# Optimization experiments

Hardware: AMD Instinct MI355X
Metric: run time of the kernel (lower is better)

## Reference

```python
import jax, jax.numpy as jnp
import numpy as np

NH = 8  # n_heads
LN_EPS = 1e-5

def _ln(x, g, b):
    m = x.mean(-1, keepdims=True)
    v = ((x - m) ** 2).mean(-1, keepdims=True)
    return (x - m) / jnp.sqrt(v + LN_EPS) * g + b

def _l2norm(x):
    n = jnp.sqrt(jnp.sum(x * x, axis=-1, keepdims=True))
    return x / jnp.maximum(n, 1e-12)

def _block(h, inw, inb, outw, outb, g1, b1, g2, b2, w1, bb1, w2, bb2):
    B, T, D = h.shape
    hd = D // NH
    res = h
    hn = _ln(h, g1, b1)
    qkv = hn @ inw.T + inb
    q, k, v = jnp.split(qkv, 3, axis=-1)
    q = q.reshape(B, T, NH, hd)
    k = k.reshape(B, T, NH, hd)
    v = v.reshape(B, T, NH, hd)
    scores = jnp.einsum('bthd,bshd->bhts', q, k) / jnp.sqrt(jnp.asarray(hd, h.dtype))
    a = jax.nn.softmax(scores, axis=-1)
    o = jnp.einsum('bhts,bshd->bthd', a, v).reshape(B, T, D)
    h = res + o @ outw.T + outb
    f = _ln(h, g2, b2)
    f = jax.nn.gelu(f @ w1.T + bb1, approximate=False) @ w2.T + bb2
    return h + f

def setup_inputs() -> dict:
    B, T, IN, D, L, NS, NP = 8, 1024, 1024, 512, 4, 1024, 512
    key = jax.random.key(0)
    ks = jax.random.split(key, 24)
    gn = jax.random.normal
    u = jax.random.uniform(ks[1], (B, T, NS), dtype=jnp.float32, minval=1e-6, maxval=1.0 - 1e-6)
    gumbel = -jnp.log(-jnp.log(u))
    s = lambda fan: 1.0 / np.sqrt(fan)
    inp = {
        'x': gn(ks[0], (B, T, IN), dtype=jnp.float32),
        'gumbel': gumbel,
        'sym_w': gn(ks[2], (D, IN)) * s(IN),
        'sym_b': jnp.zeros((D,)),
        'codebook': gn(ks[3], (NS, D)) * 0.1,
        'pos_enc': gn(ks[4], (1, 2000, D)) * 0.02,
        'attn_in_w': gn(ks[5], (L, 3 * D, D)) * s(D),
        'attn_in_b': jnp.zeros((L, 3 * D)),
        'attn_out_w': gn(ks[6], (L, D, D)) * s(D),
        'attn_out_b': jnp.zeros((L, D)),
        'n1_g': jnp.ones((L, D)), 'n1_b': jnp.zeros((L, D)),
        'n2_g': jnp.ones((L, D)), 'n2_b': jnp.zeros((L, D)),
        'ffn_w1': gn(ks[7], (L, 4 * D, D)) * s(D),
        'ffn_b1': jnp.zeros((L, 4 * D)),
        'ffn_w2': gn(ks[8], (L, D, 4 * D)) * s(4 * D),
        'ffn_b2': jnp.zeros((L, D)),
        'q_w': gn(ks[9], (D, D)) * s(D),
        'q_b': jnp.zeros((D,)),
        'qln_g': jnp.ones((D,)), 'qln_b': jnp.zeros((D,)),
        'patterns': gn(ks[10], (NP, D)) * s(D),
        'epoch': 0,
        'total_epochs': 100,
    }
    return inp

def reference(x, gumbel, sym_w, sym_b, codebook, pos_enc,
              attn_in_w, attn_in_b, attn_out_w, attn_out_b,
              n1_g, n1_b, n2_g, n2_b, ffn_w1, ffn_b1, ffn_w2, ffn_b2,
              q_w, q_b, qln_g, qln_b, patterns, epoch, total_epochs):
    B, T, _ = x.shape
    # SymbolizationLayer (soft, gumbel-softmax with tau=0.5)
    hp = x @ sym_w.T + sym_b                               # [B,T,D]
    logits_s = _l2norm(hp) @ _l2norm(codebook).T / 0.5     # [B,T,NS]
    soft = jax.nn.softmax((logits_s + gumbel) / 0.5, axis=-1)
    h = soft @ codebook + pos_enc[:, :T, :]
    # transformer blocks
    for i in range(attn_in_w.shape[0]):
        h = _block(h, attn_in_w[i], attn_in_b[i], attn_out_w[i], attn_out_b[i],
                   n1_g[i], n1_b[i], n2_g[i], n2_b[i],
                   ffn_w1[i], ffn_b1[i], ffn_w2[i], ffn_b2[i])
    # VQPatternMatrix (eval mode: hard assignments, no EMA updates)
    Q = _l2norm(_ln(h @ q_w.T + q_b, qln_g, qln_b))
    temp = max(0.5, 1.0 - 0.5 * epoch / total_epochs)
    logits = Q @ _l2norm(patterns).T / temp                # [B,T,NP]
    hard_idx = jnp.argmax(logits, axis=-1)                 # [B,T]
    assign = jax.nn.one_hot(hard_idx, patterns.shape[0], dtype=logits.dtype)
    emb = jnp.take(patterns, hard_idx, axis=0)             # gather = one_hot @ patterns
    return (emb, assign, logits, h, hard_idx)
```

## Files before the change

kernel.cpp:

```cpp
#include <hip/hip_runtime.h>

#define DEV __device__ __forceinline__

typedef unsigned short u16;
typedef unsigned int u32;
typedef __attribute__((ext_vector_type(8))) _Float16 h8_t;
typedef __attribute__((ext_vector_type(4))) float f4_t;

constexpr int T_SEQ = 1024;
constexpr int DMODEL = 512;
constexpr int NPAT = 512;

enum {
  E_BIAS = 0,
  E_VQ = 5,
  E_RES = 6,
  E_POS = 8,
  E_GUM2 = 9,
  E_GELU2 = 10,
  E_QKV2 = 11
};

DEV float h2f(u16 h) { return (float)__builtin_bit_cast(_Float16, h); }
DEV void split2(float x, u16& h, u16& l) {
  _Float16 hh = (_Float16)x;
  float r = x - (float)hh;
  _Float16 ll = (_Float16)r;
  h = __builtin_bit_cast(u16, hh);
  l = __builtin_bit_cast(u16, ll);
}

DEV f4_t mfh(h8_t a, h8_t b, f4_t c) {
  return __builtin_amdgcn_mfma_f32_16x16x32_f16(a, b, c, 0, 0, 0);
}
DEV f4_t prod3(h8_t ah, h8_t al, h8_t bh, h8_t bl, f4_t c) {
  c = mfh(ah, bh, c);
  c = mfh(ah, bl, c);
  c = mfh(al, bh, c);
  return c;
}

typedef const __attribute__((address_space(1))) unsigned char* gas_t;
typedef __attribute__((address_space(3))) unsigned char* las_t;
DEV void gload16(const u16* g, u16* l) {
  __builtin_amdgcn_global_load_lds((gas_t)(const void*)g, (las_t)(void*)l, 16,
                                   0, 0);
}

template <int EPI>
__global__ __launch_bounds__(256, 2) void gemm_mf(
    const u16* __restrict__ Ah, const u16* __restrict__ Al,
    const u16* __restrict__ Bh, const u16* __restrict__ Bl,
    const float* __restrict__ bias, const float* __restrict__ res,
    float* __restrict__ Cf, u16* __restrict__ Ch, u16* __restrict__ Cl, int N,
    int KK, int lda, int ldb, int gx) {
  __shared__ __align__(16) u16 AsH[2][128][4][8], AsL[2][128][4][8];
  __shared__ __align__(16) u16 BsH[2][128][4][8], BsL[2][128][4][8];
  const int tid = threadIdx.x;
  const int w = tid >> 6, lane = tid & 63;
  const int wy = w >> 1, wx = w & 1;
  const int lr = lane & 15, lg = lane >> 4;

  const int nwg = gridDim.x;
  const int bid = blockIdx.x;
  const int qq = nwg >> 3;
  const int wg = (bid & 7) * qq + (bid >> 3);
  const int by = wg / gx, bx = wg % gx;
  const int bm = by * 128, bn = bx * 128;

  const int rowl = lane >> 2, slot4 = lane & 3;

  auto STAGE = [&](int k0, int buf) {
#pragma unroll
    for (int it = 0; it < 4; ++it) {
      const int f = w + 4 * it;
      const int plane = f >> 3;
      const int ch = f & 7;
      const int row = ch * 16 + rowl;
      const int kp = slot4 ^ ((row >> 1) & 3);
      const size_t g = (size_t)(bm + row) * lda + k0 + kp * 8;
      if (plane == 0)
        gload16(&Ah[g], &AsH[buf][0][0][0] + ch * 512);
      else
        gload16(&Al[g], &AsL[buf][0][0][0] + ch * 512);
    }
#pragma unroll
    for (int it = 0; it < 4; ++it) {
      const int f = w + 4 * it;
      const int plane = f >> 3;
      const int ch = f & 7;
      const int row = ch * 16 + rowl;
      const int kp = slot4 ^ ((row >> 1) & 3);
      const size_t g = (size_t)(bn + row) * ldb + k0 + kp * 8;
      if (plane == 0)
        gload16(&Bh[g], &BsH[buf][0][0][0] + ch * 512);
      else
        gload16(&Bl[g], &BsL[buf][0][0][0] + ch * 512);
    }
  };

  f4_t acc[4][4];
#pragma unroll
  for (int mt = 0; mt < 4; ++mt)
#pragma unroll
    for (int nt = 0; nt < 4; ++nt) acc[mt][nt] = (f4_t){0.f, 0.f, 0.f, 0.f};

  const int nsteps = KK / 32;
  STAGE(0, 0);
  __syncthreads();
  for (int t = 0; t < nsteps; ++t) {
    const int cur = t & 1;
    if (t + 1 < nsteps) STAGE((t + 1) * 32, cur ^ 1);

    h8_t fah[4], fal[4], fbh[4], fbl[4];
#pragma unroll
    for (int mt = 0; mt < 4; ++mt) {
      int row = wy * 64 + mt * 16 + lr;
      int slot = lg ^ ((row >> 1) & 3);
      fah[mt] = *(const h8_t*)&AsH[cur][row][slot][0];
      fal[mt] = *(const h8_t*)&AsL[cur][row][slot][0];
    }
#pragma unroll
    for (int nt = 0; nt < 4; ++nt) {
      int col = wx * 64 + nt * 16 + lr;
      int slot = lg ^ ((col >> 1) & 3);
      fbh[nt] = *(const h8_t*)&BsH[cur][col][slot][0];
      fbl[nt] = *(const h8_t*)&BsL[cur][col][slot][0];
    }
#pragma unroll
    for (int mt = 0; mt < 4; ++mt)
#pragma unroll
      for (int nt = 0; nt < 4; ++nt)
        acc[mt][nt] = prod3(fah[mt], fal[mt], fbh[nt], fbl[nt], acc[mt][nt]);
    __syncthreads();
  }

  float bv[4];
  if constexpr (EPI == E_BIAS || EPI == E_RES || EPI == E_GELU2 ||
                EPI == E_QKV2) {
#pragma unroll
    for (int nt = 0; nt < 4; ++nt) bv[nt] = bias[bn + wx * 64 + nt * 16 + lr];
  }
#pragma unroll
  for (int mt = 0; mt < 4; ++mt)
#pragma unroll
    for (int nt = 0; nt < 4; ++nt) {
      const int c = bn + wx * 64 + nt * 16 + lr;
#pragma unroll
      for (int i = 0; i < 4; ++i) {
        const int m = bm + wy * 64 + mt * 16 + 4 * lg + i;
        const size_t idx = (size_t)m * N + c;
        float v = acc[mt][nt][i];
        if constexpr (EPI == E_BIAS) {
          Cf[idx] = v + bv[nt];
        } else if constexpr (EPI == E_RES) {
          Cf[idx] = v + bv[nt] + res[idx];
        } else if constexpr (EPI == E_POS) {
          Cf[idx] = v + res[(size_t)(m & 1023) * N + c];
        } else if constexpr (EPI == E_GUM2) {
          float t = 4.0f * v + 2.0f * res[idx];
          u16 h2, l2;
          split2(t, h2, l2);
          Ch[idx] = h2;
          Cl[idx] = l2;
        } else if constexpr (EPI == E_GELU2) {
          float t = v + bv[nt];
          float g = 0.5f * t * (1.0f + erff(t * 0.7071067811865476f));
          u16 h2, l2;
          split2(g, h2, l2);
          Ch[idx] = h2;
          Cl[idx] = l2;
        } else if constexpr (EPI == E_QKV2) {
          float t = v + bv[nt];
          u16 h2, l2;
          split2(t, h2, l2);
          size_t o;
          if (c < 512) {
            o = (size_t)m * 512 + c;
          } else if (c < 1024) {
            o = 4194304 + (size_t)m * 512 + (c - 512);
          } else {
            int cc = c - 1024, hh2 = cc >> 6, dd = cc & 63;
            int bb2 = m >> 10, tt = m & 1023;
            o = 8388608 +
                (((size_t)(bb2 * 8 + hh2) * 64 + dd) << 10) + tt;
          }
          Ch[o] = h2;
          Cl[o] = l2;
        }
      }
    }
}

__global__ __launch_bounds__(256, 4) void flash_mfma(
    const u16* __restrict__ QKVh, const u16* __restrict__ QKVl,
    u16* __restrict__ Oh, u16* __restrict__ Ol) {
  __shared__ __align__(16) u16 KP[2][64][8][8];
  __shared__ __align__(16) u16 Vs[2][64][8][8];
  const int tid = threadIdx.x;
  const int w = tid >> 6, lane = tid & 63;
  const int lr = lane & 15, lg = lane >> 4;
  const int bid = blockIdx.x;
  const int b = bid & 7;
  const int slot_b = bid >> 3;
  const int hh = slot_b >> 4;
  const int qt = slot_b & 15;

  const u16* Qh = QKVh;
  const u16* Ql = QKVl;
  const u16* Kh = QKVh + 4194304;
  const u16* Kl = QKVl + 4194304;
  const u16* Vh = QKVh + 8388608;
  const u16* Vl = QKVl + 8388608;

  h8_t qf[2][2];
  {
    size_t g =
        ((size_t)(b * 1024 + qt * 64 + w * 16 + lr)) * 512 + hh * 64 + lg * 8;
    qf[0][0] = *(const h8_t*)&Qh[g];
    qf[0][1] = *(const h8_t*)&Ql[g];
    qf[1][0] = *(const h8_t*)&Qh[g + 32];
    qf[1][1] = *(const h8_t*)&Ql[g + 32];
  }

  f4_t oacc[4];
#pragma unroll
  for (int nt = 0; nt < 4; ++nt) oacc[nt] = (f4_t){0.f, 0.f, 0.f, 0.f};
  float mrun[4], lrun[4];
#pragma unroll
  for (int i = 0; i < 4; ++i) {
    mrun[i] = -__builtin_huge_valf();
    lrun[i] = 0.0f;
  }

  const int rowl8 = lane >> 3, slot8 = lane & 7;

  for (int kt = 0; kt < 16; ++kt) {
    __syncthreads();
#pragma unroll
    for (int it = 0; it < 4; ++it) {
      const int f = w + 4 * it;
      const int plane = f >> 3, ch = f & 7;
      const int row = ch * 8 + rowl8;
      const int kp = slot8 ^ (row & 7);
      const size_t gk =
          ((size_t)(b * 1024 + kt * 64 + row)) * 512 + hh * 64 + kp * 8;
      if (plane == 0)
        gload16(&Kh[gk], &KP[0][0][0][0] + ch * 512);
      else
        gload16(&Kl[gk], &KP[1][0][0][0] + ch * 512);
    }
#pragma unroll
    for (int it = 0; it < 4; ++it) {
      const int f = w + 4 * it;
      const int plane = f >> 3, ch = f & 7;
      const int row = ch * 8 + rowl8;
      const int kp = slot8 ^ (row & 7);
      const size_t gv =
          ((size_t)((b * 8 + hh) * 64 + row)) * 1024 + kt * 64 + kp * 8;
      if (plane == 0)
        gload16(&Vh[gv], &Vs[0][0][0][0] + ch * 512);
      else
        gload16(&Vl[gv], &Vs[1][0][0][0] + ch * 512);
    }
    __syncthreads();

    f4_t s[4];
#pragma unroll
    for (int nt = 0; nt < 4; ++nt) {
      s[nt] = (f4_t){0.f, 0.f, 0.f, 0.f};
      const int col = nt * 16 + lr;
#pragma unroll
      for (int ks = 0; ks < 2; ++ks) {
        int slt = (ks * 4 + lg) ^ (col & 7);
        h8_t kh = *(const h8_t*)&KP[0][col][slt][0];
        h8_t kl = *(const h8_t*)&KP[1][col][slt][0];
        s[nt] = prod3(qf[ks][0], qf[ks][1], kh, kl, s[nt]);
      }
    }

#pragma unroll
    for (int i = 0; i < 4; ++i) {
      float rm = -__builtin_huge_valf();
#pragma unroll
      for (int nt = 0; nt < 4; ++nt) {
        s[nt][i] *= 0.125f;
        rm = fmaxf(rm, s[nt][i]);
      }
      rm = fmaxf(rm, __shfl_xor(rm, 1));
      rm = fmaxf(rm, __shfl_xor(rm, 2));
      rm = fmaxf(rm, __shfl_xor(rm, 4));
      rm = fmaxf(rm, __shfl_xor(rm, 8));
      float mnew = fmaxf(mrun[i], rm);
      float alpha = __expf(mrun[i] - mnew);
      float rs = 0.0f;
#pragma unroll
      for (int nt = 0; nt < 4; ++nt) {
        float p = __expf(s[nt][i] - mnew);
        s[nt][i] = p;
        rs += p;
      }
      rs += __shfl_xor(rs, 1);
      rs += __shfl_xor(rs, 2);
      rs += __shfl_xor(rs, 4);
      rs += __shfl_xor(rs, 8);
      lrun[i] = lrun[i] * alpha + rs;
      mrun[i] = mnew;
#pragma unroll
      for (int nt = 0; nt < 4; ++nt) oacc[nt][i] *= alpha;
    }

    __syncthreads();

#pragma unroll
    for (int nt = 0; nt < 4; ++nt)
#pragma unroll
      for (int i = 0; i < 4; ++i) {
        int qrow = w * 16 + 4 * lg + i;
        int kv = nt * 16 + lr;
        int kp = kv >> 3, j = kv & 7;
        int slt = kp ^ (qrow & 7);
        u16 h2, l2;
        split2(s[nt][i], h2, l2);
        KP[0][qrow][slt][j] = h2;
        KP[1][qrow][slt][j] = l2;
      }

    h8_t pf[2][2];
#pragma unroll
    for (int ks = 0; ks < 2; ++ks) {
      int row = w * 16 + lr;
      int slt = (ks * 4 + lg) ^ (row & 7);
      pf[ks][0] = *(const h8_t*)&KP[0][row][slt][0];
      pf[ks][1] = *(const h8_t*)&KP[1][row][slt][0];
    }
#pragma unroll
    for (int ntd = 0; ntd < 4; ++ntd) {
      const int col = ntd * 16 + lr;
#pragma unroll
      for (int ks = 0; ks < 2; ++ks) {
        int slt = (ks * 4 + lg) ^ (col & 7);
        h8_t vh = *(const h8_t*)&Vs[0][col][slt][0];
        h8_t vl = *(const h8_t*)&Vs[1][col][slt][0];
        oacc[ntd] = prod3(pf[ks][0], pf[ks][1], vh, vl, oacc[ntd]);
      }
    }
  }

#pragma unroll
  for (int i = 0; i < 4; ++i) {
    float inv = 1.0f / lrun[i];
    int t = qt * 64 + w * 16 + 4 * lg + i;
#pragma unroll
    for (int ntd = 0; ntd < 4; ++ntd) {
      int d = hh * 64 + ntd * 16 + lr;
      size_t idx = ((size_t)(b * 1024 + t)) * 512 + d;
      u16 h2, l2;
      split2(oacc[ntd][i] * inv, h2, l2);
      Oh[idx] = h2;
      Ol[idx] = l2;
    }
  }
}

template <int BM, int BN, int WR, int EPI>
__global__ __launch_bounds__((BM / WR) * (BN / 64) * 64) void gemm_f32(
    const float* __restrict__ A, const float* __restrict__ Bmat,
    const float* __restrict__ bias, float* __restrict__ C, int M, int N, int K,
    const int* __restrict__ ep, const int* __restrict__ tot) {
  constexpr int BK = 16;
  constexpr int WN = BN / 64;
  constexpr int NW = (BM / WR) * WN;
  constexpr int NT = NW * 64;
  constexpr int RM = WR / 8;
  __shared__ __align__(16) float As[BK][BM + 4];
  __shared__ __align__(16) float Bs[BK][BN + 4];
  const int tid = threadIdx.x;
  const int w = tid >> 6, lane = tid & 63;
  const int wy = w / WN, wx = w % WN;
  const int ly = lane >> 3, lx = lane & 7;
  const int bm = blockIdx.y * BM;
  const int bn = blockIdx.x * BN;
  const int rbase = wy * WR + ly * RM;

  float acc[RM][8];
#pragma unroll
  for (int i = 0; i < RM; ++i)
#pragma unroll
    for (int j = 0; j < 8; ++j) acc[i][j] = 0.0f;

  for (int k0 = 0; k0 < K; k0 += BK) {
#pragma unroll
    for (int i = 0; i < (BM * BK / 4) / NT; ++i) {
      int idx = tid + i * NT;
      int r = idx >> 2, c4 = (idx & 3) << 2;
      const float4 v = *(const float4*)(A + (size_t)(bm + r) * K + k0 + c4);
      As[c4 + 0][r] = v.x;
      As[c4 + 1][r] = v.y;
      As[c4 + 2][r] = v.z;
      As[c4 + 3][r] = v.w;
    }
#pragma unroll
    for (int i = 0; i < (BN * BK / 4) / NT; ++i) {
      int idx = tid + i * NT;
      int r = idx >> 2, c4 = (idx & 3) << 2;
      const float4 v = *(const float4*)(Bmat + (size_t)(bn + r) * K + k0 + c4);
      Bs[c4 + 0][r] = v.x;
      Bs[c4 + 1][r] = v.y;
      Bs[c4 + 2][r] = v.z;
      Bs[c4 + 3][r] = v.w;
    }
    __syncthreads();
#pragma unroll
    for (int k = 0; k < BK; ++k) {
      float a[RM], b[8];
#pragma unroll
      for (int r4 = 0; r4 < RM; r4 += 4)
        *(float4*)&a[r4] = *(const float4*)&As[k][rbase + r4];
      *(float4*)&b[0] = *(const float4*)&Bs[k][wx * 64 + lx * 8];
      *(float4*)&b[4] = *(const float4*)&Bs[k][wx * 64 + lx * 8 + 4];
#pragma unroll
      for (int i = 0; i < RM; ++i)
#pragma unroll
        for (int j = 0; j < 8; ++j) acc[i][j] = fmaf(a[i], b[j], acc[i][j]);
    }
    __syncthreads();
  }

  const int ncol = bn + wx * 64 + lx * 8;
  float bb[8];
  if constexpr (EPI == E_BIAS) {
    *(float4*)&bb[0] = *(const float4*)(bias + ncol);
    *(float4*)&bb[4] = *(const float4*)(bias + ncol + 4);
  }
  float invt = 1.0f;
  if constexpr (EPI == E_VQ) {
    float t = 1.0f - 0.5f * (float)ep[0] / (float)tot[0];
    invt = 1.0f / fmaxf(0.5f, t);
  }
#pragma unroll
  for (int i = 0; i < RM; ++i) {
    const int m = bm + rbase + i;
    float o[8];
#pragma unroll
    for (int j = 0; j < 8; ++j) o[j] = acc[i][j];
    if constexpr (EPI == E_BIAS) {
#pragma unroll
      for (int j = 0; j < 8; ++j) o[j] += bb[j];
    } else if constexpr (EPI == E_VQ) {
#pragma unroll
      for (int j = 0; j < 8; ++j) o[j] *= invt;
    }
    *(float4*)(C + (size_t)m * N + ncol) = *(float4*)&o[0];
    *(float4*)(C + (size_t)m * N + ncol + 4) = *(float4*)&o[4];
  }
}

DEV float wave_sum(float v) {
#pragma unroll
  for (int off = 1; off < 64; off <<= 1) v += __shfl_xor(v, off);
  return v;
}

DEV void store8_split2(u16* H, u16* L, size_t base, const float* t) {
  u16 vh[8], vl[8];
#pragma unroll
  for (int j = 0; j < 8; ++j) split2(t[j], vh[j], vl[j]);
  *(ushort4*)&H[base] = make_ushort4(vh[0], vh[1], vh[2], vh[3]);
  *(ushort4*)&H[base + 4] = make_ushort4(vh[4], vh[5], vh[6], vh[7]);
  *(ushort4*)&L[base] = make_ushort4(vl[0], vl[1], vl[2], vl[3]);
  *(ushort4*)&L[base + 4] = make_ushort4(vl[4], vl[5], vl[6], vl[7]);
}

__global__ __launch_bounds__(256) void ln_split2(const float* __restrict__ x,
                                                 const float* __restrict__ g,
                                                 const float* __restrict__ b,
                                                 u16* __restrict__ yh,
                                                 u16* __restrict__ yl) {
  const int row = blockIdx.x * 4 + (threadIdx.x >> 6);
  const int lane = threadIdx.x & 63;
  const float* xr = x + (size_t)row * DMODEL;
  float v[8];
  *(float4*)&v[0] = *(const float4*)(xr + lane * 8);
  *(float4*)&v[4] = *(const float4*)(xr + lane * 8 + 4);
  float s = 0.0f;
#pragma unroll
  for (int j = 0; j < 8; ++j) s += v[j];
  s = wave_sum(s);
  float mean = s * (1.0f / 512.0f);
  float s2 = 0.0f;
#pragma unroll
  for (int j = 0; j < 8; ++j) {
    float d = v[j] - mean;
    s2 += d * d;
  }
  s2 = wave_sum(s2);
  float rstd = 1.0f / sqrtf(s2 * (1.0f / 512.0f) + 1e-5f);
  float gg[8], bv[8];
  *(float4*)&gg[0] = *(const float4*)(g + lane * 8);
  *(float4*)&gg[4] = *(const float4*)(g + lane * 8 + 4);
  *(float4*)&bv[0] = *(const float4*)(b + lane * 8);
  *(float4*)&bv[4] = *(const float4*)(b + lane * 8 + 4);
  float t[8];
#pragma unroll
  for (int j = 0; j < 8; ++j) t[j] = (v[j] - mean) * rstd * gg[j] + bv[j];
  store8_split2(yh, yl, (size_t)row * DMODEL + lane * 8, t);
}

__global__ __launch_bounds__(256) void ln_l2_f32(const float* __restrict__ x,
                                                 const float* __restrict__ g,
                                                 const float* __restrict__ b,
                                                 float* __restrict__ y) {
  const int row = blockIdx.x * 4 + (threadIdx.x >> 6);
  const int lane = threadIdx.x & 63;
  const float* xr = x + (size_t)row * DMODEL;
  float v[8];
  *(float4*)&v[0] = *(const float4*)(xr + lane * 8);
  *(float4*)&v[4] = *(const float4*)(xr + lane * 8 + 4);
  float s = 0.0f;
#pragma unroll
  for (int j = 0; j < 8; ++j) s += v[j];
  s = wave_sum(s);
  float mean = s * (1.0f / 512.0f);
  float s2 = 0.0f;
#pragma unroll
  for (int j = 0; j < 8; ++j) {
    float d = v[j] - mean;
    s2 += d * d;
  }
  s2 = wave_sum(s2);
  float rstd = 1.0f / sqrtf(s2 * (1.0f / 512.0f) + 1e-5f);
  float gg[8], bv[8];
  *(float4*)&gg[0] = *(const float4*)(g + lane * 8);
  *(float4*)&gg[4] = *(const float4*)(g + lane * 8 + 4);
  *(float4*)&bv[0] = *(const float4*)(b + lane * 8);
  *(float4*)&bv[4] = *(const float4*)(b + lane * 8 + 4);
  float t[8];
#pragma unroll
  for (int j = 0; j < 8; ++j) t[j] = (v[j] - mean) * rstd * gg[j] + bv[j];
  float n2 = 0.0f;
#pragma unroll
  for (int j = 0; j < 8; ++j) n2 += t[j] * t[j];
  n2 = wave_sum(n2);
  float den = fmaxf(sqrtf(n2), 1e-12f);
#pragma unroll
  for (int j = 0; j < 8; ++j) t[j] /= den;
  float* yr = y + (size_t)row * DMODEL;
  *(float4*)(yr + lane * 8) = *(float4*)&t[0];
  *(float4*)(yr + lane * 8 + 4) = *(float4*)&t[4];
}

__global__ __launch_bounds__(256) void l2_split2(const float* __restrict__ x,
                                                 u16* __restrict__ yh,
                                                 u16* __restrict__ yl) {
  const int row = blockIdx.x * 4 + (threadIdx.x >> 6);
  const int lane = threadIdx.x & 63;
  const float* xr = x + (size_t)row * DMODEL;
  float v[8];
  *(float4*)&v[0] = *(const float4*)(xr + lane * 8);
  *(float4*)&v[4] = *(const float4*)(xr + lane * 8 + 4);
  float n2 = 0.0f;
#pragma unroll
  for (int j = 0; j < 8; ++j) n2 += v[j] * v[j];
  n2 = wave_sum(n2);
  float den = fmaxf(sqrtf(n2), 1e-12f);
#pragma unroll
  for (int j = 0; j < 8; ++j) v[j] /= den;
  store8_split2(yh, yl, (size_t)row * DMODEL + lane * 8, v);
}

__global__ __launch_bounds__(256) void l2_f32(const float* __restrict__ x,
                                              float* __restrict__ y) {
  const int row = blockIdx.x * 4 + (threadIdx.x >> 6);
  const int lane = threadIdx.x & 63;
  const float* xr = x + (size_t)row * DMODEL;
  float v[8];
  *(float4*)&v[0] = *(const float4*)(xr + lane * 8);
  *(float4*)&v[4] = *(const float4*)(xr + lane * 8 + 4);
  float n2 = 0.0f;
#pragma unroll
  for (int j = 0; j < 8; ++j) n2 += v[j] * v[j];
  n2 = wave_sum(n2);
  float den = fmaxf(sqrtf(n2), 1e-12f);
#pragma unroll
  for (int j = 0; j < 8; ++j) v[j] /= den;
  float* yr = y + (size_t)row * DMODEL;
  *(float4*)(yr + lane * 8) = *(float4*)&v[0];
  *(float4*)(yr + lane * 8 + 4) = *(float4*)&v[4];
}

__global__ __launch_bounds__(256) void softmax2(u16* __restrict__ H,
                                                u16* __restrict__ L) {
  const int row = blockIdx.x;
  const int tid = threadIdx.x;
  const size_t base = (size_t)row * 1024 + tid * 4;
  ushort4 qh = *(const ushort4*)&H[base];
  ushort4 ql = *(const ushort4*)&L[base];
  float v0 = h2f(qh.x) + h2f(ql.x);
  float v1 = h2f(qh.y) + h2f(ql.y);
  float v2 = h2f(qh.z) + h2f(ql.z);
  float v3 = h2f(qh.w) + h2f(ql.w);
  float mx = fmaxf(fmaxf(v0, v1), fmaxf(v2, v3));
#pragma unroll
  for (int off = 1; off < 64; off <<= 1) mx = fmaxf(mx, __shfl_xor(mx, off));
  __shared__ float red[4];
  const int wv = tid >> 6;
  if ((tid & 63) == 0) red[wv] = mx;
  __syncthreads();
  mx = fmaxf(fmaxf(red[0], red[1]), fmaxf(red[2], red[3]));
  float e0 = __expf(v0 - mx), e1 = __expf(v1 - mx), e2 = __expf(v2 - mx),
        e3 = __expf(v3 - mx);
  float s = e0 + e1 + e2 + e3;
#pragma unroll
  for (int off = 1; off < 64; off <<= 1) s += __shfl_xor(s, off);
  __syncthreads();
  if ((tid & 63) == 0) red[wv] = s;
  __syncthreads();
  s = red[0] + red[1] + red[2] + red[3];
  float inv = 1.0f / s;
  u16 ah[4], al[4];
  split2(e0 * inv, ah[0], al[0]);
  split2(e1 * inv, ah[1], al[1]);
  split2(e2 * inv, ah[2], al[2]);
  split2(e3 * inv, ah[3], al[3]);
  *(ushort4*)&H[base] = make_ushort4(ah[0], ah[1], ah[2], ah[3]);
  *(ushort4*)&L[base] = make_ushort4(al[0], al[1], al[2], al[3]);
}

__global__ __launch_bounds__(256) void split2_k(const float* __restrict__ src,
                                                u16* __restrict__ H,
                                                u16* __restrict__ L, int n4) {
  for (int e = blockIdx.x * 256 + threadIdx.x; e < n4; e += gridDim.x * 256) {
    float4 v = *(const float4*)(src + (size_t)e * 4);
    u16 ah[4], al[4];
    split2(v.x, ah[0], al[0]);
    split2(v.y, ah[1], al[1]);
    split2(v.z, ah[2], al[2]);
    split2(v.w, ah[3], al[3]);
    *(ushort4*)&H[(size_t)e * 4] = make_ushort4(ah[0], ah[1], ah[2], ah[3]);
    *(ushort4*)&L[(size_t)e * 4] = make_ushort4(al[0], al[1], al[2], al[3]);
  }
}

__global__ __launch_bounds__(256) void tsplit_cb(const float* __restrict__ cb,
                                                 u16* __restrict__ th,
                                                 u16* __restrict__ tl) {
  const int c = blockIdx.x;
  const int t = threadIdx.x;
  u16 ah[4], al[4];
#pragma unroll
  for (int j = 0; j < 4; ++j) {
    float v = cb[(size_t)(4 * t + j) * 512 + c];
    split2(v, ah[j], al[j]);
  }
  const size_t base = (size_t)c * 1024 + 4 * t;
  *(ushort4*)&th[base] = make_ushort4(ah[0], ah[1], ah[2], ah[3]);
  *(ushort4*)&tl[base] = make_ushort4(al[0], al[1], al[2], al[3]);
}

__global__ __launch_bounds__(256) void vq_finalize(
    const float* __restrict__ logits, const float* __restrict__ patterns,
    float* __restrict__ emb, float* __restrict__ assign,
    float* __restrict__ idxf) {
  const int row = blockIdx.x * 4 + (threadIdx.x >> 6);
  const int lane = threadIdx.x & 63;
  const float* lr = logits + (size_t)row * NPAT;
  float best = -__builtin_huge_valf();
  int bi = 0;
#pragma unroll
  for (int jj = 0; jj < 8; ++jj) {
    int j = lane + jj * 64;
    float v = lr[j];
    if (v > best) {
      best = v;
      bi = j;
    }
  }
#pragma unroll
  for (int off = 1; off < 64; off <<= 1) {
    float ob = __shfl_xor(best, off);
    int oi = __shfl_xor(bi, off);
    if (ob > best || (ob == best && oi < bi)) {
      best = ob;
      bi = oi;
    }
  }
  const float* pr = patterns + (size_t)bi * DMODEL;
#pragma unroll
  for (int g = 0; g < 2; ++g) {
    int c = lane * 8 + g * 4;
    float4 pv = *(const float4*)(pr + c);
    *(float4*)(emb + (size_t)row * DMODEL + c) = pv;
    float4 av;
    av.x = (c + 0 == bi) ? 1.0f : 0.0f;
    av.y = (c + 1 == bi) ? 1.0f : 0.0f;
    av.z = (c + 2 == bi) ? 1.0f : 0.0f;
    av.w = (c + 3 == bi) ? 1.0f : 0.0f;
    *(float4*)(assign + (size_t)row * NPAT + c) = av;
  }
  if (lane == 0) idxf[row] = (float)bi;
}

extern "C" void kernel_launch(void* const* d_in, const int* in_sizes, int n_in,
                              void* d_out, int out_size, void* d_ws,
                              size_t ws_size, hipStream_t stream) {
  (void)in_sizes;
  (void)n_in;
  (void)out_size;
  (void)ws_size;
  const float* x = (const float*)d_in[0];
  const float* gumbel = (const float*)d_in[1];
  const float* sym_w = (const float*)d_in[2];
  const float* sym_b = (const float*)d_in[3];
  const float* codebook = (const float*)d_in[4];
  const float* pos_enc = (const float*)d_in[5];
  const float* attn_in_w = (const float*)d_in[6];
  const float* attn_in_b = (const float*)d_in[7];
  const float* attn_out_w = (const float*)d_in[8];
  const float* attn_out_b = (const float*)d_in[9];
  const float* n1_g = (const float*)d_in[10];
  const float* n1_b = (const float*)d_in[11];
  const float* n2_g = (const float*)d_in[12];
  const float* n2_b = (const float*)d_in[13];
  const float* ffn_w1 = (const float*)d_in[14];
  const float* ffn_b1 = (const float*)d_in[15];
  const float* ffn_w2 = (const float*)d_in[16];
  const float* ffn_b2 = (const float*)d_in[17];
  const float* q_w = (const float*)d_in[18];
  const float* q_b = (const float*)d_in[19];
  const float* qln_g = (const float*)d_in[20];
  const float* qln_b = (const float*)d_in[21];
  const float* patterns = (const float*)d_in[22];
  const int* epoch = (const int*)d_in[23];
  const int* tot = (const int*)d_in[24];

  float* out = (float*)d_out;
  float* emb = out;
  float* assign = out + 4194304;
  float* logits = out + 8388608;
  float* h = out + 12582912;
  float* idxf = out + 16777216;

  float* ws_f = (float*)d_ws;
  u16* a16 = (u16*)ws_f;
  float* bF = ws_f + 18874368;
  u16* b16 = (u16*)bF;
  u16 *hnH = b16, *hnL = b16 + 4194304;
  float* wF = ws_f + 25165824;
  u16* w16 = (u16*)wF;

  u16 *xH = a16, *xL = a16 + 8388608;
  split2_k<<<2048, 256, 0, stream>>>(x, xH, xL, 2097152);
  split2_k<<<512, 256, 0, stream>>>(sym_w, w16, w16 + 524288, 131072);
  gemm_mf<E_BIAS><<<256, 256, 0, stream>>>(xH, xL, w16, w16 + 524288, sym_b,
                                           nullptr, bF, nullptr, nullptr, 512,
                                           1024, 1024, 1024, 4);
  l2_split2<<<256, 256, 0, stream>>>(codebook, w16, w16 + 524288);
  u16 *hpH = a16, *hpL = a16 + 4194304;
  l2_split2<<<2048, 256, 0, stream>>>(bF, hpH, hpL);
  u16 *sH = a16 + 12582912, *sL = a16 + 20971520;
  gemm_mf<E_GUM2><<<512, 256, 0, stream>>>(hpH, hpL, w16, w16 + 524288,
                                           nullptr, gumbel, nullptr, sH, sL,
                                           1024, 512, 512, 512, 8);
  softmax2<<<8192, 256, 0, stream>>>(sH, sL);
  tsplit_cb<<<512, 256, 0, stream>>>(codebook, w16, w16 + 524288);
  gemm_mf<E_POS><<<256, 256, 0, stream>>>(sH, sL, w16, w16 + 524288, nullptr,
                                          pos_enc, h, nullptr, nullptr, 512,
                                          1024, 1024, 1024, 4);

  u16 *qkvH = a16, *qkvL = a16 + 12582912;
  u16* w1p = a16 + 33554432;
  u16* w2p = b16 + 8388608;
  u16 *pH = a16, *pL = a16 + 16777216;

  for (int l = 0; l < 4; ++l) {
    const float* inw = attn_in_w + (size_t)l * 1536 * 512;
    const float* inb = attn_in_b + (size_t)l * 1536;
    const float* outw = attn_out_w + (size_t)l * 512 * 512;
    const float* outb = attn_out_b + (size_t)l * 512;
    const float* w1 = ffn_w1 + (size_t)l * 2048 * 512;
    const float* b1 = ffn_b1 + (size_t)l * 2048;
    const float* w2 = ffn_w2 + (size_t)l * 512 * 2048;
    const float* b2 = ffn_b2 + (size_t)l * 512;

    ln_split2<<<2048, 256, 0, stream>>>(h, n1_g + l * 512, n1_b + l * 512,
                                        hnH, hnL);
    split2_k<<<1024, 256, 0, stream>>>(inw, w16, w16 + 786432, 196608);
    gemm_mf<E_QKV2><<<768, 256, 0, stream>>>(hnH, hnL, w16, w16 + 786432, inb,
                                             nullptr, nullptr, qkvH, qkvL,
                                             1536, 512, 512, 512, 12);
    flash_mfma<<<1024, 256, 0, stream>>>(qkvH, qkvL, hnH, hnL);
    split2_k<<<256, 256, 0, stream>>>(outw, w16, w16 + 262144, 65536);
    gemm_mf<E_RES><<<256, 256, 0, stream>>>(hnH, hnL, w16, w16 + 262144, outb,
                                            h, h, nullptr, nullptr, 512, 512,
                                            512, 512, 4);
    ln_split2<<<2048, 256, 0, stream>>>(h, n2_g + l * 512, n2_b + l * 512,
                                        hnH, hnL);
    split2_k<<<1024, 256, 0, stream>>>(w1, w1p, w1p + 1048576, 262144);
    split2_k<<<1024, 256, 0, stream>>>(w2, w2p, w2p + 1048576, 262144);
    gemm_mf<E_GELU2><<<1024, 256, 0, stream>>>(hnH, hnL, w1p, w1p + 1048576,
                                               b1, nullptr, nullptr, pH, pL,
                                               2048, 512, 512, 512, 16);
    gemm_mf<E_RES><<<256, 256, 0, stream>>>(pH, pL, w2p, w2p + 1048576, b2, h,
                                            h, nullptr, nullptr, 512, 2048,
                                            2048, 2048, 4);
  }

  gemm_f32<64, 128, 32, E_BIAS><<<dim3(4, 128), 256, 0, stream>>>(
      h, q_w, q_b, bF, 8192, 512, 512, nullptr, nullptr);
  ln_l2_f32<<<2048, 256, 0, stream>>>(bF, qln_g, qln_b, bF);
  l2_f32<<<128, 256, 0, stream>>>(patterns, wF);
  gemm_f32<64, 128, 32, E_VQ><<<dim3(4, 128), 256, 0, stream>>>(
      bF, wF, nullptr, logits, 8192, 512, 512, epoch, tot);
  vq_finalize<<<2048, 256, 0, stream>>>(logits, patterns, emb, assign, idxf);
}
```

Before: 1.766 ms.

## Use BM=64 MFMA tiles for narrow GEMMs and move VQ head onto split-fp16 MFMA

Templates the split-fp16 MFMA GEMM on row-tile height, so the N=512 GEMMs (symbolization, gumbel, pos, out-proj, FFN2) launch twice as many 64-row blocks for better CU fill. It also replaces the scalar fp32 GEMMs of the final VQ projection and pattern logits with the split-fp16 MFMA GEMM, adding split kernels and a temperature-scaling epilogue. This risks small precision differences in the logits and argmax that depend on the three-product fp16 split emulation.

```diff
diff --git a/kernel.cpp b/kernel.cpp
--- a/kernel.cpp
+++ b/kernel.cpp
@@ -47,14 +47,17 @@
                                    0, 0);
 }
 
-template <int EPI>
-__global__ __launch_bounds__(256, 2) void gemm_mf(
+template <int BM, int EPI>
+__global__ __launch_bounds__(256, BM == 64 ? 3 : 2) void gemm_mf(
     const u16* __restrict__ Ah, const u16* __restrict__ Al,
     const u16* __restrict__ Bh, const u16* __restrict__ Bl,
     const float* __restrict__ bias, const float* __restrict__ res,
     float* __restrict__ Cf, u16* __restrict__ Ch, u16* __restrict__ Cl, int N,
-    int KK, int lda, int ldb, int gx) {
-  __shared__ __align__(16) u16 AsH[2][128][4][8], AsL[2][128][4][8];
+    int KK, int lda, int ldb, int gx, const int* __restrict__ ep,
+    const int* __restrict__ tot) {
+  constexpr int MT = BM / 32;
+  constexpr int CPP = BM / 16;
+  __shared__ __align__(16) u16 AsH[2][BM][4][8], AsL[2][BM][4][8];
   __shared__ __align__(16) u16 BsH[2][128][4][8], BsL[2][128][4][8];
   const int tid = threadIdx.x;
   const int w = tid >> 6, lane = tid & 63;
@@ -66,16 +69,16 @@
   const int qq = nwg >> 3;
   const int wg = (bid & 7) * qq + (bid >> 3);
   const int by = wg / gx, bx = wg % gx;
-  const int bm = by * 128, bn = bx * 128;
+  const int bm = by * BM, bn = bx * 128;
 
   const int rowl = lane >> 2, slot4 = lane & 3;
 
   auto STAGE = [&](int k0, int buf) {
 #pragma unroll
-    for (int it = 0; it < 4; ++it) {
+    for (int it = 0; it < CPP / 2; ++it) {
       const int f = w + 4 * it;
-      const int plane = f >> 3;
-      const int ch = f & 7;
+      const int plane = f / CPP;
+      const int ch = f % CPP;
       const int row = ch * 16 + rowl;
       const int kp = slot4 ^ ((row >> 1) & 3);
       const size_t g = (size_t)(bm + row) * lda + k0 + kp * 8;
@@ -99,9 +102,9 @@
     }
   };
 
-  f4_t acc[4][4];
-#pragma unroll
-  for (int mt = 0; mt < 4; ++mt)
+  f4_t acc[MT][4];
+#pragma unroll
+  for (int mt = 0; mt < MT; ++mt)
 #pragma unroll
     for (int nt = 0; nt < 4; ++nt) acc[mt][nt] = (f4_t){0.f, 0.f, 0.f, 0.f};
 
@@ -112,10 +115,10 @@
     const int cur = t & 1;
     if (t + 1 < nsteps) STAGE((t + 1) * 32, cur ^ 1);
 
-    h8_t fah[4], fal[4], fbh[4], fbl[4];
-#pragma unroll
-    for (int mt = 0; mt < 4; ++mt) {
-      int row = wy * 64 + mt * 16 + lr;
+    h8_t fah[MT], fal[MT], fbh[4], fbl[4];
+#pragma unroll
+    for (int mt = 0; mt < MT; ++mt) {
+      int row = wy * (BM / 2) + mt * 16 + lr;
       int slot = lg ^ ((row >> 1) & 3);
       fah[mt] = *(const h8_t*)&AsH[cur][row][slot][0];
       fal[mt] = *(const h8_t*)&AsL[cur][row][slot][0];
@@ -128,7 +131,7 @@
       fbl[nt] = *(const h8_t*)&BsL[cur][col][slot][0];
     }
 #pragma unroll
-    for (int mt = 0; mt < 4; ++mt)
+    for (int mt = 0; mt < MT; ++mt)
 #pragma unroll
       for (int nt = 0; nt < 4; ++nt)
         acc[mt][nt] = prod3(fah[mt], fal[mt], fbh[nt], fbl[nt], acc[mt][nt]);
@@ -141,18 +144,25 @@
 #pragma unroll
     for (int nt = 0; nt < 4; ++nt) bv[nt] = bias[bn + wx * 64 + nt * 16 + lr];
   }
-#pragma unroll
-  for (int mt = 0; mt < 4; ++mt)
+  float invt = 1.0f;
+  if constexpr (EPI == E_VQ) {
+    float tt = 1.0f - 0.5f * (float)ep[0] / (float)tot[0];
+    invt = 1.0f / fmaxf(0.5f, tt);
+  }
+#pragma unroll
+  for (int mt = 0; mt < MT; ++mt)
 #pragma unroll
     for (int nt = 0; nt < 4; ++nt) {
       const int c = bn + wx * 64 + nt * 16 + lr;
 #pragma unroll
       for (int i = 0; i < 4; ++i) {
-        const int m = bm + wy * 64 + mt * 16 + 4 * lg + i;
+        const int m = bm + wy * (BM / 2) + mt * 16 + 4 * lg + i;
         const size_t idx = (size_t)m * N + c;
         float v = acc[mt][nt][i];
         if constexpr (EPI == E_BIAS) {
           Cf[idx] = v + bv[nt];
+        } else if constexpr (EPI == E_VQ) {
+          Cf[idx] = v * invt;
         } else if constexpr (EPI == E_RES) {
           Cf[idx] = v + bv[nt] + res[idx];
         } else if constexpr (EPI == E_POS) {
@@ -181,9 +191,9 @@
             o = 4194304 + (size_t)m * 512 + (c - 512);
           } else {
             int cc = c - 1024, hh2 = cc >> 6, dd = cc & 63;
-            int bb2 = m >> 10, tt = m & 1023;
+            int bb2 = m >> 10, tt2 = m & 1023;
             o = 8388608 +
-                (((size_t)(bb2 * 8 + hh2) * 64 + dd) << 10) + tt;
+                (((size_t)(bb2 * 8 + hh2) * 64 + dd) << 10) + tt2;
           }
           Ch[o] = h2;
           Cl[o] = l2;
@@ -363,99 +373,6 @@
   }
 }
 
-template <int BM, int BN, int WR, int EPI>
-__global__ __launch_bounds__((BM / WR) * (BN / 64) * 64) void gemm_f32(
-    const float* __restrict__ A, const float* __restrict__ Bmat,
-    const float* __restrict__ bias, float* __restrict__ C, int M, int N, int K,
-    const int* __restrict__ ep, const int* __restrict__ tot) {
-  constexpr int BK = 16;
-  constexpr int WN = BN / 64;
-  constexpr int NW = (BM / WR) * WN;
-  constexpr int NT = NW * 64;
-  constexpr int RM = WR / 8;
-  __shared__ __align__(16) float As[BK][BM + 4];
-  __shared__ __align__(16) float Bs[BK][BN + 4];
-  const int tid = threadIdx.x;
-  const int w = tid >> 6, lane = tid & 63;
-  const int wy = w / WN, wx = w % WN;
-  const int ly = lane >> 3, lx = lane & 7;
-  const int bm = blockIdx.y * BM;
-  const int bn = blockIdx.x * BN;
-  const int rbase = wy * WR + ly * RM;
-
-  float acc[RM][8];
-#pragma unroll
-  for (int i = 0; i < RM; ++i)
-#pragma unroll
-    for (int j = 0; j < 8; ++j) acc[i][j] = 0.0f;
-
-  for (int k0 = 0; k0 < K; k0 += BK) {
-#pragma unroll
-    for (int i = 0; i < (BM * BK / 4) / NT; ++i) {
-      int idx = tid + i * NT;
-      int r = idx >> 2, c4 = (idx & 3) << 2;
-      const float4 v = *(const float4*)(A + (size_t)(bm + r) * K + k0 + c4);
-      As[c4 + 0][r] = v.x;
-      As[c4 + 1][r] = v.y;
-      As[c4 + 2][r] = v.z;
-      As[c4 + 3][r] = v.w;
-    }
-#pragma unroll
-    for (int i = 0; i < (BN * BK / 4) / NT; ++i) {
-      int idx = tid + i * NT;
-      int r = idx >> 2, c4 = (idx & 3) << 2;
-      const float4 v = *(const float4*)(Bmat + (size_t)(bn + r) * K + k0 + c4);
-      Bs[c4 + 0][r] = v.x;
-      Bs[c4 + 1][r] = v.y;
-      Bs[c4 + 2][r] = v.z;
-      Bs[c4 + 3][r] = v.w;
-    }
-    __syncthreads();
-#pragma unroll
-    for (int k = 0; k < BK; ++k) {
-      float a[RM], b[8];
-#pragma unroll
-      for (int r4 = 0; r4 < RM; r4 += 4)
-        *(float4*)&a[r4] = *(const float4*)&As[k][rbase + r4];
-      *(float4*)&b[0] = *(const float4*)&Bs[k][wx * 64 + lx * 8];
-      *(float4*)&b[4] = *(const float4*)&Bs[k][wx * 64 + lx * 8 + 4];
-#pragma unroll
-      for (int i = 0; i < RM; ++i)
-#pragma unroll
-        for (int j = 0; j < 8; ++j) acc[i][j] = fmaf(a[i], b[j], acc[i][j]);
-    }
-    __syncthreads();
-  }
-
-  const int ncol = bn + wx * 64 + lx * 8;
-  float bb[8];
-  if constexpr (EPI == E_BIAS) {
-    *(float4*)&bb[0] = *(const float4*)(bias + ncol);
-    *(float4*)&bb[4] = *(const float4*)(bias + ncol + 4);
-  }
-  float invt = 1.0f;
-  if constexpr (EPI == E_VQ) {
-    float t = 1.0f - 0.5f * (float)ep[0] / (float)tot[0];
-    invt = 1.0f / fmaxf(0.5f, t);
-  }
-#pragma unroll
-  for (int i = 0; i < RM; ++i) {
-    const int m = bm + rbase + i;
-    float o[8];
-#pragma unroll
-    for (int j = 0; j < 8; ++j) o[j] = acc[i][j];
-    if constexpr (EPI == E_BIAS) {
-#pragma unroll
-      for (int j = 0; j < 8; ++j) o[j] += bb[j];
-    } else if constexpr (EPI == E_VQ) {
-#pragma unroll
-      for (int j = 0; j < 8; ++j) o[j] *= invt;
-    }
-    *(float4*)(C + (size_t)m * N + ncol) = *(float4*)&o[0];
-    *(float4*)(C + (size_t)m * N + ncol + 4) = *(float4*)&o[4];
-  }
-}
-
 DEV float wave_sum(float v) {
 #pragma unroll
   for (int off = 1; off < 64; off <<= 1) v += __shfl_xor(v, off);
@@ -507,10 +424,9 @@
   store8_split2(yh, yl, (size_t)row * DMODEL + lane * 8, t);
 }
 
-__global__ __launch_bounds__(256) void ln_l2_f32(const float* __restrict__ x,
-                                                 const float* __restrict__ g,
-                                                 const float* __restrict__ b,
-                                                 float* __restrict__ y) {
+__global__ __launch_bounds__(256) void ln_l2_split2(
+    const float* __restrict__ x, const float* __restrict__ g,
+    const float* __restrict__ b, u16* __restrict__ yh, u16* __restrict__ yl) {
   const int row = blockIdx.x * 4 + (threadIdx.x >> 6);
   const int lane = threadIdx.x & 63;
   const float* xr = x + (size_t)row * DMODEL;
@@ -545,9 +461,7 @@
   float den = fmaxf(sqrtf(n2), 1e-12f);
 #pragma unroll
   for (int j = 0; j < 8; ++j) t[j] /= den;
-  float* yr = y + (size_t)row * DMODEL;
-  *(float4*)(yr + lane * 8) = *(float4*)&t[0];
-  *(float4*)(yr + lane * 8 + 4) = *(float4*)&t[4];
+  store8_split2(yh, yl, (size_t)row * DMODEL + lane * 8, t);
 }
 
 __global__ __launch_bounds__(256) void l2_split2(const float* __restrict__ x,
@@ -567,26 +481,6 @@
 #pragma unroll
   for (int j = 0; j < 8; ++j) v[j] /= den;
   store8_split2(yh, yl, (size_t)row * DMODEL + lane * 8, v);
-}
-
-__global__ __launch_bounds__(256) void l2_f32(const float* __restrict__ x,
-                                              float* __restrict__ y) {
-  const int row = blockIdx.x * 4 + (threadIdx.x >> 6);
-  const int lane = threadIdx.x & 63;
-  const float* xr = x + (size_t)row * DMODEL;
-  float v[8];
-  *(float4*)&v[0] = *(const float4*)(xr + lane * 8);
-  *(float4*)&v[4] = *(const float4*)(xr + lane * 8 + 4);
-  float n2 = 0.0f;
-#pragma unroll
-  for (int j = 0; j < 8; ++j) n2 += v[j] * v[j];
-  n2 = wave_sum(n2);
-  float den = fmaxf(sqrtf(n2), 1e-12f);
-#pragma unroll
-  for (int j = 0; j < 8; ++j) v[j] /= den;
-  float* yr = y + (size_t)row * DMODEL;
-  *(float4*)(yr + lane * 8) = *(float4*)&v[0];
-  *(float4*)(yr + lane * 8 + 4) = *(float4*)&v[4];
 }
 
 __global__ __launch_bounds__(256) void softmax2(u16* __restrict__ H,
@@ -752,21 +646,21 @@
   u16 *xH = a16, *xL = a16 + 8388608;
   split2_k<<<2048, 256, 0, stream>>>(x, xH, xL, 2097152);
   split2_k<<<512, 256, 0, stream>>>(sym_w, w16, w16 + 524288, 131072);
-  gemm_mf<E_BIAS><<<256, 256, 0, stream>>>(xH, xL, w16, w16 + 524288, sym_b,
-                                           nullptr, bF, nullptr, nullptr, 512,
-                                           1024, 1024, 1024, 4);
+  gemm_mf<64, E_BIAS><<<512, 256, 0, stream>>>(
+      xH, xL, w16, w16 + 524288, sym_b, nullptr, bF, nullptr, nullptr, 512,
+      1024, 1024, 1024, 4, nullptr, nullptr);
   l2_split2<<<256, 256, 0, stream>>>(codebook, w16, w16 + 524288);
   u16 *hpH = a16, *hpL = a16 + 4194304;
   l2_split2<<<2048, 256, 0, stream>>>(bF, hpH, hpL);
   u16 *sH = a16 + 12582912, *sL = a16 + 20971520;
-  gemm_mf<E_GUM2><<<512, 256, 0, stream>>>(hpH, hpL, w16, w16 + 524288,
-                                           nullptr, gumbel, nullptr, sH, sL,
-                                           1024, 512, 512, 512, 8);
+  gemm_mf<64, E_GUM2><<<1024, 256, 0, stream>>>(
+      hpH, hpL, w16, w16 + 524288, nullptr, gumbel, nullptr, sH, sL, 1024, 512,
+      512, 512, 8, nullptr, nullptr);
   softmax2<<<8192, 256, 0, stream>>>(sH, sL);
   tsplit_cb<<<512, 256, 0, stream>>>(codebook, w16, w16 + 524288);
-  gemm_mf<E_POS><<<256, 256, 0, stream>>>(sH, sL, w16, w16 + 524288, nullptr,
-                                          pos_enc, h, nullptr, nullptr, 512,
-                                          1024, 1024, 1024, 4);
+  gemm_mf<64, E_POS><<<512, 256, 0, stream>>>(
+      sH, sL, w16, w16 + 524288, nullptr, pos_enc, h, nullptr, nullptr, 512,
+      1024, 1024, 1024, 4, nullptr, nullptr);
 
   u16 *qkvH = a16, *qkvL = a16 + 12582912;
   u16* w1p = a16 + 33554432;
@@ -786,31 +680,37 @@
     ln_split2<<<2048, 256, 0, stream>>>(h, n1_g + l * 512, n1_b + l * 512,
                                         hnH, hnL);
     split2_k<<<1024, 256, 0, stream>>>(inw, w16, w16 + 786432, 196608);
-    gemm_mf<E_QKV2><<<768, 256, 0, stream>>>(hnH, hnL, w16, w16 + 786432, inb,
-                                             nullptr, nullptr, qkvH, qkvL,
-                                             1536, 512, 512, 512, 12);
+    gemm_mf<128, E_QKV2><<<768, 256, 0, stream>>>(
+        hnH, hnL, w16, w16 + 786432, inb, nullptr, nullptr, qkvH, qkvL, 1536,
+        512, 512, 512, 12, nullptr, nullptr);
     flash_mfma<<<1024, 256, 0, stream>>>(qkvH, qkvL, hnH, hnL);
     split2_k<<<256, 256, 0, stream>>>(outw, w16, w16 + 262144, 65536);
-    gemm_mf<E_RES><<<256, 256, 0, stream>>>(hnH, hnL, w16, w16 + 262144, outb,
-                                            h, h, nullptr, nullptr, 512, 512,
-                                            512, 512, 4);
+    gemm_mf<64, E_RES><<<512, 256, 0, stream>>>(
+        hnH, hnL, w16, w16 + 262144, outb, h, h, nullptr, nullptr, 512, 512,
+        512, 512, 4, nullptr, nullptr);
     ln_split2<<<2048, 256, 0, stream>>>(h, n2_g + l * 512, n2_b + l * 512,
                                         hnH, hnL);
     split2_k<<<1024, 256, 0, stream>>>(w1, w1p, w1p + 1048576, 262144);
     split2_k<<<1024, 256, 0, stream>>>(w2, w2p, w2p + 1048576, 262144);
-    gemm_mf<E_GELU2><<<1024, 256, 0, stream>>>(hnH, hnL, w1p, w1p + 1048576,
-                                               b1, nullptr, nullptr, pH, pL,
-                                               2048, 512, 512, 512, 16);
-    gemm_mf<E_RES><<<256, 256, 0, stream>>>(pH, pL, w2p, w2p + 1048576, b2, h,
-                                            h, nullptr, nullptr, 512, 2048,
-                                            2048, 2048, 4);
-  }
-
-  gemm_f32<64, 128, 32, E_BIAS><<<dim3(4, 128), 256, 0, stream>>>(
-      h, q_w, q_b, bF, 8192, 512, 512, nullptr, nullptr);
-  ln_l2_f32<<<2048, 256, 0, stream>>>(bF, qln_g, qln_b, bF);
-  l2_f32<<<128, 256, 0, stream>>>(patterns, wF);
-  gemm_f32<64, 128, 32, E_VQ><<<dim3(4, 128), 256, 0, stream>>>(
-      bF, wF, nullptr, logits, 8192, 512, 512, epoch, tot);
+    gemm_mf<128, E_GELU2><<<1024, 256, 0, stream>>>(
+        hnH, hnL, w1p, w1p + 1048576, b1, nullptr, nullptr, pH, pL, 2048, 512,
+        512, 512, 16, nullptr, nullptr);
+    gemm_mf<64, E_RES><<<512, 256, 0, stream>>>(
+        pH, pL, w2p, w2p + 1048576, b2, h, h, nullptr, nullptr, 512, 2048,
+        2048, 2048, 4, nullptr, nullptr);
+  }
+
+  u16 *hsH = a16, *hsL = a16 + 4194304;
+  u16 *QpH = a16 + 8388608, *QpL = a16 + 12582912;
+  split2_k<<<1024, 256, 0, stream>>>(h, hsH, hsL, 1048576);
+  split2_k<<<256, 256, 0, stream>>>(q_w, w16, w16 + 262144, 65536);
+  gemm_mf<64, E_BIAS><<<512, 256, 0, stream>>>(
+      hsH, hsL, w16, w16 + 262144, q_b, nullptr, bF, nullptr, nullptr, 512,
+      512, 512, 512, 4, nullptr, nullptr);
+  ln_l2_split2<<<2048, 256, 0, stream>>>(bF, qln_g, qln_b, QpH, QpL);
+  l2_split2<<<128, 256, 0, stream>>>(patterns, w16 + 524288, w16 + 786432);
+  gemm_mf<64, E_VQ><<<512, 256, 0, stream>>>(
+      QpH, QpL, w16 + 524288, w16 + 786432, nullptr, nullptr, logits, nullptr,
+      nullptr, 512, 512, 512, 512, 4, epoch, tot);
   vq_finalize<<<2048, 256, 0, stream>>>(logits, patterns, emb, assign, idxf);
 }
```

New measurement: 1.618 ms (median of 2 runs). 1.09x faster.
